# Optimization experiments

Hardware: AMD Instinct MI355X
Metric: run time of the kernel (lower is better)

## Reference

```python
import jax, jax.numpy as jnp
import numpy as np

NUM_HEADS = 16
LN_EPS = 1e-5
RMS_EPS = 1e-6


def rmsnorm(x, gamma, eps=RMS_EPS):
    xf = x.astype(jnp.float32)
    rms = jax.lax.rsqrt(jnp.mean(xf * xf, axis=-1, keepdims=True) + eps)
    return gamma * (xf * rms).astype(x.dtype)


def layernorm(x, g, b, eps=LN_EPS):
    mu = jnp.mean(x, axis=-1, keepdims=True)
    var = jnp.mean(jnp.square(x - mu), axis=-1, keepdims=True)
    return (x - mu) * jax.lax.rsqrt(var + eps) * g + b


def setup_inputs() -> dict:
    key = jax.random.key(0)
    E = 2048
    ks = jax.random.split(key, 10)
    std = 0.02
    inp = {
        "x": jax.random.normal(ks[0], (2, 2048, E), dtype=jnp.float32),
        "Wq": jax.random.normal(ks[1], (E, E), dtype=jnp.float32) * std,
        "Wk": jax.random.normal(ks[2], (E, E), dtype=jnp.float32) * std,
        "Wv": jax.random.normal(ks[3], (E, E), dtype=jnp.float32) * std,
        "Wo": jax.random.normal(ks[4], (E, E), dtype=jnp.float32) * std,
        "ln_g": jnp.ones((E,), jnp.float32),
        "ln_b": jnp.zeros((E,), jnp.float32),
        "rms_g": jnp.ones((E,), jnp.float32),
        "mlp_W0": jax.random.normal(ks[5], (E, E), dtype=jnp.float32) * std,
        "sw_W": jax.random.normal(ks[6], (E, E), dtype=jnp.float32) * std,
        "sw_V": jax.random.normal(ks[7], (E, E), dtype=jnp.float32) * std,
        "sw_beta": jnp.ones((1,), jnp.float32),
        "mlp_rms_g": jnp.ones((E,), jnp.float32),
    }
    return inp


def reference(x, Wq, Wk, Wv, Wo, ln_g, ln_b, rms_g, mlp_W0, sw_W, sw_V, sw_beta, mlp_rms_g):
    B, S, E = x.shape
    H = NUM_HEADS
    Dh = E // H
    scale = 1.0 / (Dh ** 0.5)

    # --- MultiheadAttention (faithful to original einsum/view quirks) ---
    q = x @ Wq.T                     # (B,S,E)
    k = (x @ Wk.T) * scale
    v = x @ Wv.T
    qh = q.reshape(B, S, H, Dh)
    kh = k.reshape(B, S, H, Dh)
    scores = jnp.einsum('bthd,bshd->bhts', qh, kh)        # (B,H,T,S)
    causal = jnp.tril(jnp.ones((S, S), dtype=bool))
    scores = jnp.where(causal, scores, -jnp.inf)
    attn = jax.nn.softmax(scores, axis=-1)
    # NOTE: v is split (B,S,Dh,H) -- head/head_dim axes swapped vs q/k, as in the torch code
    vh = v.reshape(B, S, Dh, H)
    ctx = jnp.einsum('bsdh,bhts->bthd', vh, attn)          # == torch 'kjlm,kmij->kiml'
    ctx = ctx.reshape(B, S, E)                              # flatten heads-major
    ctx = layernorm(ctx, ln_g, ln_b)
    attn_out = ctx @ Wo.T

    x = x + attn_out
    x = rmsnorm(x, rms_g)

    # --- MLP: Linear -> SwiGLU -> RMSNorm, residual ---
    h = x @ mlp_W0.T
    w = h @ sw_W.T
    swish = w * jax.nn.sigmoid(sw_beta * w)
    g = swish * (h @ sw_V.T)
    mlp_out = rmsnorm(g, mlp_rms_g)
    return x + mlp_out
```

## Files before the change

kernel.cpp:

```cpp
#include <hip/hip_runtime.h>


#define B_    2
#define S_    2048
#define E_    2048
#define H_    16
#define DH    128
#define MROWS 4096
#define NEGF  (-3.0e38f)

typedef unsigned short ushort_t;
typedef unsigned int   uint_t;
typedef ushort_t us8   __attribute__((ext_vector_type(8)));
typedef ushort_t us4   __attribute__((ext_vector_type(4)));
typedef __bf16   bf16x8 __attribute__((ext_vector_type(8)));
typedef float    f32x4 __attribute__((ext_vector_type(4)));

__device__ __forceinline__ float b2f(ushort_t u) {
    uint_t x = ((uint_t)u) << 16;
    union { uint_t u; float f; } c; c.u = x; return c.f;
}
__device__ __forceinline__ ushort_t f2b(float f) {
    union { float f; uint_t u; } c; c.f = f;
    uint_t x = c.u;
    uint_t r = (x + 0x7fffu + ((x >> 16) & 1u)) >> 16;
    return (ushort_t)r;
}
__device__ __forceinline__ float fexp2(float x) {
    return __builtin_amdgcn_exp2f(x);
}

__device__ __forceinline__ void gld16(const ushort_t* g, ushort_t* l) {
    __builtin_amdgcn_global_load_lds(
        (const __attribute__((address_space(1))) void*)g,
        (__attribute__((address_space(3))) void*)l,
        16, 0, 0);
}

__global__ void probe_dtype(const ushort_t* w, int* flag) {
    __shared__ int cnt;
    if (threadIdx.x == 0) cnt = 0;
    __syncthreads();
    int c = 0;
    for (int i = threadIdx.x; i < 4096; i += 256) {
        uint_t e = (w[i] >> 7) & 0xFFu;
        if (e >= 0x84u) c++;
    }
    atomicAdd(&cnt, c);
    __syncthreads();
    if (threadIdx.x == 0) *flag = (cnt >= 8) ? 1 : 0;
}

__global__ void convert_k(const void* src, ushort_t* dst, long n, const int* flag) {
    int f = *flag;
    long i0 = (long)blockIdx.x * blockDim.x + threadIdx.x;
    long stride = (long)gridDim.x * blockDim.x;
    long n4 = n >> 2;
    if (f) {
        const f32x4* s = (const f32x4*)src;
        for (long i = i0; i < n4; i += stride) {
            f32x4 v = s[i];
            us4 o = { f2b(v[0]), f2b(v[1]), f2b(v[2]), f2b(v[3]) };
            *(us4*)(dst + i * 4) = o;
        }
        for (long i = n4 * 4 + i0; i < n; i += stride)
            dst[i] = f2b(((const float*)src)[i]);
    } else {
        const us4* s = (const us4*)src;
        for (long i = i0; i < n4; i += stride)
            *(us4*)(dst + i * 4) = s[i];
        for (long i = n4 * 4 + i0; i < n; i += stride)
            dst[i] = ((const ushort_t*)src)[i];
    }
}

__global__ void fill_diag(float* out, long n, float val) {
    long i = (long)blockIdx.x * 256 + threadIdx.x;
    if (i < n) out[i] = val;
}

__global__ __launch_bounds__(256) void gemm_bt(
    const ushort_t* __restrict__ A, const ushort_t* __restrict__ W,
    ushort_t* out, const ushort_t* resid, const ushort_t* beta,
    void* outv, const int* flagp, float scale, int mode)
{
    const int K = E_, N = E_;
    __shared__ alignas(16) ushort_t Asf[128 * 32];
    __shared__ alignas(16) ushort_t Bsf[128 * 32];

    const int tid  = threadIdx.x;
    const int wave = tid >> 6;
    const int lane = tid & 63;
    const int wm   = (wave >> 1) * 64;
    const int wn   = (wave & 1) * 64;
    const int lrow = lane & 15;
    const int quad = lane >> 4;
    const int m0   = blockIdx.y * 128;
    const int n0   = blockIdx.x * 128;

    const float betav = (beta != nullptr) ? b2f(beta[0]) : 0.0f;
    const int   of32  = (flagp != nullptr) ? *flagp : 0;

    f32x4 acc[4][4];
#pragma unroll
    for (int i = 0; i < 4; i++)
#pragma unroll
        for (int j = 0; j < 4; j++) acc[i][j] = f32x4{0.f, 0.f, 0.f, 0.f};

    const int ch   = wave * 2;
    const int crow = lane >> 2;
    const int ccol = (lane & 3) * 8;
    const ushort_t* Ag0 = A + (long)(m0 + ch * 16 + crow) * K + ccol;
    const ushort_t* Wg0 = W + (long)(n0 + ch * 16 + crow) * K + ccol;
    ushort_t* Al0 = &Asf[ch * 16 * 32];
    ushort_t* Bl0 = &Bsf[ch * 16 * 32];

    for (int kk = 0; kk < K; kk += 32) {
        gld16(Ag0 + kk,          Al0);
        gld16(Ag0 + 16 * K + kk, Al0 + 512);
        gld16(Wg0 + kk,          Bl0);
        gld16(Wg0 + 16 * K + kk, Bl0 + 512);
        __syncthreads();

        bf16x8 af[4], bfr[4];
#pragma unroll
        for (int i = 0; i < 4; i++)
            af[i]  = __builtin_bit_cast(bf16x8, *(const us8*)&Asf[(wm + i*16 + lrow) * 32 + quad * 8]);
#pragma unroll
        for (int j = 0; j < 4; j++)
            bfr[j] = __builtin_bit_cast(bf16x8, *(const us8*)&Bsf[(wn + j*16 + lrow) * 32 + quad * 8]);
#pragma unroll
        for (int i = 0; i < 4; i++)
#pragma unroll
            for (int j = 0; j < 4; j++)
                acc[i][j] = __builtin_amdgcn_mfma_f32_16x16x32_bf16(af[i], bfr[j], acc[i][j], 0, 0, 0);
        __syncthreads();
    }

#pragma unroll
    for (int i = 0; i < 4; i++)
#pragma unroll
        for (int j = 0; j < 4; j++)
#pragma unroll
            for (int r = 0; r < 4; r++) {
                int m = m0 + wm + i*16 + quad*4 + r;
                int n = n0 + wn + j*16 + lrow;
                float v = acc[i][j][r] * scale;
                long idx;
                if (mode == 1) {
                    int h = n >> 7, d = n & 127;
                    idx = ((long)h * S_ + m) * DH + d;
                } else if (mode == 2) {
                    int d = n >> 4, h = n & 15;
                    idx = ((long)h * DH + d) * S_ + m;
                } else {
                    idx = (long)m * N + n;
                    if (mode == 3) {
                        v += b2f(resid[idx]);
                    } else if (mode == 4) {
                        float wv  = b2f(resid[idx]);
                        float sig = 1.0f / (1.0f + expf(-betav * wv));
                        v = wv * sig * v;
                        if (of32) { ((float*)outv)[idx] = v; continue; }
                    }
                }
                out[idx] = f2b(v);
            }
}

__global__ __launch_bounds__(256) void gemm_qkv(
    const ushort_t* __restrict__ X,
    const ushort_t* __restrict__ Wq, const ushort_t* __restrict__ Wk,
    const ushort_t* __restrict__ Wv,
    ushort_t* qo, ushort_t* ko, ushort_t* vo, float kscale)
{
    const int K = E_;
    __shared__ alignas(16) ushort_t Asf[128 * 32];
    __shared__ alignas(16) ushort_t Bsf[128 * 32];

    const int tid  = threadIdx.x;
    const int wave = tid >> 6;
    const int lane = tid & 63;
    const int wm   = (wave >> 1) * 64;
    const int wn   = (wave & 1) * 64;
    const int lrow = lane & 15;
    const int quad = lane >> 4;
    const int sel  = blockIdx.x >> 4;
    const int n0   = (blockIdx.x & 15) * 128;
    const int m0   = blockIdx.y * 128;
    const long zoff = (long)blockIdx.z * ((long)S_ * E_);

    const ushort_t* A = X + zoff;
    const ushort_t* W = (sel == 0) ? Wq : (sel == 1) ? Wk : Wv;
    const float scale = (sel == 1) ? kscale : 1.0f;
    ushort_t* out = ((sel == 0) ? qo : (sel == 1) ? ko : vo) + zoff;

    f32x4 acc[4][4];
#pragma unroll
    for (int i = 0; i < 4; i++)
#pragma unroll
        for (int j = 0; j < 4; j++) acc[i][j] = f32x4{0.f, 0.f, 0.f, 0.f};

    const int ch   = wave * 2;
    const int crow = lane >> 2;
    const int ccol = (lane & 3) * 8;
    const ushort_t* Ag0 = A + (long)(m0 + ch * 16 + crow) * K + ccol;
    const ushort_t* Wg0 = W + (long)(n0 + ch * 16 + crow) * K + ccol;
    ushort_t* Al0 = &Asf[ch * 16 * 32];
    ushort_t* Bl0 = &Bsf[ch * 16 * 32];

    for (int kk = 0; kk < K; kk += 32) {
        gld16(Ag0 + kk,          Al0);
        gld16(Ag0 + 16 * K + kk, Al0 + 512);
        gld16(Wg0 + kk,          Bl0);
        gld16(Wg0 + 16 * K + kk, Bl0 + 512);
        __syncthreads();

        bf16x8 af[4], bfr[4];
#pragma unroll
        for (int i = 0; i < 4; i++)
            af[i]  = __builtin_bit_cast(bf16x8, *(const us8*)&Asf[(wm + i*16 + lrow) * 32 + quad * 8]);
#pragma unroll
        for (int j = 0; j < 4; j++)
            bfr[j] = __builtin_bit_cast(bf16x8, *(const us8*)&Bsf[(wn + j*16 + lrow) * 32 + quad * 8]);
#pragma unroll
        for (int i = 0; i < 4; i++)
#pragma unroll
            for (int j = 0; j < 4; j++)
                acc[i][j] = __builtin_amdgcn_mfma_f32_16x16x32_bf16(af[i], bfr[j], acc[i][j], 0, 0, 0);
        __syncthreads();
    }

#pragma unroll
    for (int i = 0; i < 4; i++)
#pragma unroll
        for (int j = 0; j < 4; j++)
#pragma unroll
            for (int r = 0; r < 4; r++) {
                int m = m0 + wm + i*16 + quad*4 + r;
                int n = n0 + wn + j*16 + lrow;
                float v = acc[i][j][r] * scale;
                long idx;
                if (sel <= 1) {
                    int h = n >> 7, d = n & 127;
                    idx = ((long)h * S_ + m) * DH + d;
                } else {
                    int d = n >> 4, h = n & 15;
                    idx = ((long)h * DH + d) * S_ + m;
                }
                out[idx] = f2b(v);
            }
}

__global__ __launch_bounds__(256) void flash_attn(
    const ushort_t* __restrict__ qp, const ushort_t* __restrict__ kp,
    const ushort_t* __restrict__ vt, ushort_t* ctx)
{
    __shared__ alignas(16) ushort_t Kt[64][144];
    __shared__ alignas(16) ushort_t Vt[128][72];
    __shared__ alignas(16) ushort_t Pb[4][16][72];

    const long zq = (long)blockIdx.z * ((long)S_ * E_);
    qp  += zq; kp += zq; vt += zq; ctx += zq;

    const int tid  = threadIdx.x;
    const int wave = tid >> 6;
    const int lane = tid & 63;
    const int lrow = lane & 15;
    const int quad = lane >> 4;
    const int h    = blockIdx.y;

    const long qbase = (long)h * S_ * DH;
    const long vbase = (long)h * DH * S_;

    int kr[4], kc[4], vr[4], vc[4];
#pragma unroll
    for (int it = 0; it < 4; it++) {
        int L = tid + it * 256;
        kr[it] = L >> 4; kc[it] = (L & 15) * 8;
        vr[it] = L >> 3; vc[it] = (L & 7) * 8;
    }

#pragma unroll 1
    for (int half = 0; half < 2; half++) {
        const int qt = (half == 0) ? (int)blockIdx.x : (31 - (int)blockIdx.x);
        const int tw = qt * 64 + wave * 16;

        bf16x8 qf[4];
        {
            const ushort_t* qrow = qp + qbase + (long)(tw + lrow) * DH + quad * 8;
#pragma unroll
            for (int ks = 0; ks < 4; ks++)
                qf[ks] = __builtin_bit_cast(bf16x8, *(const us8*)(qrow + ks * 32));
        }

        float m_i[4], l_i[4];
#pragma unroll
        for (int r = 0; r < 4; r++) { m_i[r] = NEGF; l_i[r] = 0.0f; }
        f32x4 o[8];
#pragma unroll
        for (int i = 0; i < 8; i++) o[i] = f32x4{0.f, 0.f, 0.f, 0.f};

        us8 kreg[4], vreg[4];
#pragma unroll
        for (int it = 0; it < 4; it++)
            kreg[it] = *(const us8*)(kp + qbase + (long)kr[it] * DH + kc[it]);
#pragma unroll
        for (int it = 0; it < 4; it++)
            vreg[it] = *(const us8*)(vt + vbase + (long)vr[it] * S_ + vc[it]);

        for (int st = 0; st <= qt; st++) {
            const int sb = st * 64;

#pragma unroll
            for (int it = 0; it < 4; it++) *(us8*)&Kt[kr[it]][kc[it]] = kreg[it];
#pragma unroll
            for (int it = 0; it < 4; it++) *(us8*)&Vt[vr[it]][vc[it]] = vreg[it];
            __syncthreads();

            if (st < qt) {
                const int sb2 = sb + 64;
#pragma unroll
                for (int it = 0; it < 4; it++)
                    kreg[it] = *(const us8*)(kp + qbase + (long)(sb2 + kr[it]) * DH + kc[it]);
#pragma unroll
                for (int it = 0; it < 4; it++)
                    vreg[it] = *(const us8*)(vt + vbase + (long)vr[it] * S_ + sb2 + vc[it]);
            }

            f32x4 sacc[4];
#pragma unroll
            for (int nt = 0; nt < 4; nt++) {
                sacc[nt] = f32x4{0.f, 0.f, 0.f, 0.f};
#pragma unroll
                for (int ks = 0; ks < 4; ks++) {
                    bf16x8 kf = __builtin_bit_cast(bf16x8, *(const us8*)&Kt[nt*16 + lrow][ks*32 + quad*8]);
                    sacc[nt] = __builtin_amdgcn_mfma_f32_16x16x32_bf16(qf[ks], kf, sacc[nt], 0, 0, 0);
                }
            }

            const bool diag = (st == qt);
            float alpha[4];
#pragma unroll
            for (int r = 0; r < 4; r++) {
                const int trow = tw + quad * 4 + r;
                float pv[4];
#pragma unroll
                for (int nt = 0; nt < 4; nt++) {
                    float sv = sacc[nt][r];
                    if (diag && (sb + nt*16 + lrow > trow)) sv = NEGF;
                    pv[nt] = sv;
                }
                float mx = fmaxf(fmaxf(pv[0], pv[1]), fmaxf(pv[2], pv[3]));
                mx = fmaxf(mx, __shfl_xor(mx, 1));
                mx = fmaxf(mx, __shfl_xor(mx, 2));
                mx = fmaxf(mx, __shfl_xor(mx, 4));
                mx = fmaxf(mx, __shfl_xor(mx, 8));
                float mn = fmaxf(m_i[r], mx);
                float al = fexp2(m_i[r] - mn);
                float s  = 0.0f;
#pragma unroll
                for (int nt = 0; nt < 4; nt++) {
                    float p = fexp2(pv[nt] - mn);
                    s += p;
                    Pb[wave][quad*4 + r][nt*16 + lrow] = f2b(p);
                }
                s += __shfl_xor(s, 1);
                s += __shfl_xor(s, 2);
                s += __shfl_xor(s, 4);
                s += __shfl_xor(s, 8);
                l_i[r]  = l_i[r] * al + s;
                m_i[r]  = mn;
                alpha[r] = al;
            }
#pragma unroll
            for (int nt = 0; nt < 8; nt++)
#pragma unroll
                for (int r = 0; r < 4; r++) o[nt][r] *= alpha[r];

            bf16x8 pf[2];
#pragma unroll
            for (int ks = 0; ks < 2; ks++)
                pf[ks] = __builtin_bit_cast(bf16x8, *(const us8*)&Pb[wave][lrow][ks*32 + quad*8]);
#pragma unroll
            for (int nt = 0; nt < 8; nt++)
#pragma unroll
                for (int ks = 0; ks < 2; ks++) {
                    bf16x8 vf = __builtin_bit_cast(bf16x8, *(const us8*)&Vt[nt*16 + lrow][ks*32 + quad*8]);
                    o[nt] = __builtin_amdgcn_mfma_f32_16x16x32_bf16(pf[ks], vf, o[nt], 0, 0, 0);
                }
            __syncthreads();
        }

        float li4[4];
#pragma unroll
        for (int r = 0; r < 4; r++) li4[r] = 1.0f / l_i[r];
#pragma unroll
        for (int nt = 0; nt < 8; nt++)
#pragma unroll
            for (int r = 0; r < 4; r++) {
                int t = tw + quad*4 + r;
                int d = nt*16 + lrow;
                ctx[(long)t * E_ + h * DH + d] = f2b(o[nt][r] * li4[r]);
            }
    }
}

__global__ __launch_bounds__(256) void ln_rows(
    const ushort_t* x, const ushort_t* __restrict__ g,
    const ushort_t* __restrict__ bta, ushort_t* out)
{
    __shared__ float red[16];
    const int row = blockIdx.x;
    const ushort_t* xr = x + (long)row * E_;
    float vals[8], s = 0.f, ss = 0.f;
#pragma unroll
    for (int i = 0; i < 8; i++) {
        float v = b2f(xr[threadIdx.x + i * 256]);
        vals[i] = v; s += v; ss += v * v;
    }
    for (int off = 1; off < 64; off <<= 1) { s += __shfl_xor(s, off); ss += __shfl_xor(ss, off); }
    int wave = threadIdx.x >> 6, lane = threadIdx.x & 63;
    if (lane == 0) { red[wave] = s; red[8 + wave] = ss; }
    __syncthreads();
    if (threadIdx.x == 0) {
        red[4]  = red[0] + red[1] + red[2] + red[3];
        red[12] = red[8] + red[9] + red[10] + red[11];
    }
    __syncthreads();
    float mu  = red[4] / E_;
    float var = red[12] / E_ - mu * mu;
    float rs  = rsqrtf(var + 1e-5f);
#pragma unroll
    for (int i = 0; i < 8; i++) {
        int c = threadIdx.x + i * 256;
        float v = (vals[i] - mu) * rs * b2f(g[c]) + b2f(bta[c]);
        out[(long)row * E_ + c] = f2b(v);
    }
}

__global__ __launch_bounds__(256) void rms_rows(
    const ushort_t* x, const ushort_t* __restrict__ g, ushort_t* out)
{
    __shared__ float red[8];
    const int row = blockIdx.x;
    const ushort_t* xr = x + (long)row * E_;
    float vals[8], ss = 0.f;
#pragma unroll
    for (int i = 0; i < 8; i++) {
        float v = b2f(xr[threadIdx.x + i * 256]);
        vals[i] = v; ss += v * v;
    }
    for (int off = 1; off < 64; off <<= 1) ss += __shfl_xor(ss, off);
    int wave = threadIdx.x >> 6, lane = threadIdx.x & 63;
    if (lane == 0) red[wave] = ss;
    __syncthreads();
    if (threadIdx.x == 0) red[4] = red[0] + red[1] + red[2] + red[3];
    __syncthreads();
    float rms = rsqrtf(red[4] / E_ + 1e-6f);
#pragma unroll
    for (int i = 0; i < 8; i++) {
        int c = threadIdx.x + i * 256;
        float v = b2f(f2b(vals[i] * rms)) * b2f(g[c]);
        out[(long)row * E_ + c] = f2b(v);
    }
}

__global__ __launch_bounds__(256) void rms_final(
    const void* x, const ushort_t* __restrict__ g,
    const ushort_t* resid, void* outv, const int* flagp)
{
    __shared__ float red[8];
    const int row = blockIdx.x;
    const int of32 = *flagp;
    float vals[8], ss = 0.f;
#pragma unroll
    for (int i = 0; i < 8; i++) {
        int c = threadIdx.x + i * 256;
        float v = of32 ? ((const float*)x)[(long)row * E_ + c]
                       : b2f(((const ushort_t*)x)[(long)row * E_ + c]);
        vals[i] = v; ss += v * v;
    }
    for (int off = 1; off < 64; off <<= 1) ss += __shfl_xor(ss, off);
    int wave = threadIdx.x >> 6, lane = threadIdx.x & 63;
    if (lane == 0) red[wave] = ss;
    __syncthreads();
    if (threadIdx.x == 0) red[4] = red[0] + red[1] + red[2] + red[3];
    __syncthreads();
    float rms = rsqrtf(red[4] / E_ + 1e-6f);
#pragma unroll
    for (int i = 0; i < 8; i++) {
        int c = threadIdx.x + i * 256;
        long idx = (long)row * E_ + c;
        if (of32) {
            float v = vals[i] * rms * b2f(g[c]) + b2f(resid[idx]);
            ((float*)outv)[idx] = v;
        } else {
            float v = b2f(f2b(vals[i] * rms)) * b2f(g[c]) + b2f(resid[idx]);
            ((ushort_t*)outv)[idx] = f2b(v);
        }
    }
}

extern "C" void kernel_launch(void* const* d_in, const int* in_sizes, int n_in,
                              void* d_out, int out_size, void* d_ws, size_t ws_size,
                              hipStream_t stream)
{
    const size_t NB  = (size_t)MROWS * E_;
    const size_t WSZ = (size_t)E_ * E_;
    const size_t QSZ = (size_t)S_ * E_;
    const float kscale = 0.08838834764831845f * 1.4426950408889634f;

    const size_t stage_elems = NB + 7 * WSZ + 6 * 4096;
    const size_t need_def    = (stage_elems + 2 * NB) * 2;
    const size_t need_direct = 2 * NB * 2;

    dim3 gFull(E_ / 128, MROWS / 128);

    if (ws_size >= need_def) {
        ushort_t* st = (ushort_t*)d_ws;
        ushort_t* c_x   = st;
        ushort_t* c_Wq  = c_x  + NB;
        ushort_t* c_Wk  = c_Wq + WSZ;
        ushort_t* c_Wv  = c_Wk + WSZ;
        ushort_t* c_Wo  = c_Wv + WSZ;
        ushort_t* c_W0  = c_Wo + WSZ;
        ushort_t* c_sW  = c_W0 + WSZ;
        ushort_t* c_sV  = c_sW + WSZ;
        ushort_t* c_lng = c_sV + WSZ;
        ushort_t* c_lnb = c_lng + 4096;
        ushort_t* c_rg  = c_lnb + 4096;
        ushort_t* c_mg  = c_rg  + 4096;
        ushort_t* c_sb  = c_mg  + 4096;
        int*      flag  = (int*)(c_sb + 4096);
        ushort_t* w0    = st + stage_elems;
        ushort_t* w1    = w0 + NB;
        ushort_t* ob    = (ushort_t*)d_out;
        ushort_t* ob2   = ob + NB;

        probe_dtype<<<1, 256, 0, stream>>>((const ushort_t*)d_in[1], flag);
        convert_k<<<1024, 256, 0, stream>>>(d_in[0],  c_x,  (long)NB,  flag);
        convert_k<<<1024, 256, 0, stream>>>(d_in[1],  c_Wq, (long)WSZ, flag);
        convert_k<<<1024, 256, 0, stream>>>(d_in[2],  c_Wk, (long)WSZ, flag);
        convert_k<<<1024, 256, 0, stream>>>(d_in[3],  c_Wv, (long)WSZ, flag);
        convert_k<<<1024, 256, 0, stream>>>(d_in[4],  c_Wo, (long)WSZ, flag);
        convert_k<<<1024, 256, 0, stream>>>(d_in[8],  c_W0, (long)WSZ, flag);
        convert_k<<<1024, 256, 0, stream>>>(d_in[9],  c_sW, (long)WSZ, flag);
        convert_k<<<1024, 256, 0, stream>>>(d_in[10], c_sV, (long)WSZ, flag);
        convert_k<<<8,    256, 0, stream>>>(d_in[5],  c_lng, E_, flag);
        convert_k<<<8,    256, 0, stream>>>(d_in[6],  c_lnb, E_, flag);
        convert_k<<<8,    256, 0, stream>>>(d_in[7],  c_rg,  E_, flag);
        convert_k<<<8,    256, 0, stream>>>(d_in[12], c_mg,  E_, flag);
        convert_k<<<1,    64,  0, stream>>>(d_in[11], c_sb,  1,  flag);

        gemm_qkv<<<dim3(48, 16, 2), 256, 0, stream>>>(c_x, c_Wq, c_Wk, c_Wv,
                                                      w0, ob, w1, kscale);
        flash_attn<<<dim3(16, H_, 2), 256, 0, stream>>>(w0, ob, w1, ob2);

        ln_rows<<<MROWS, 256, 0, stream>>>(ob2, c_lng, c_lnb, ob2);
        gemm_bt<<<gFull, 256, 0, stream>>>(ob2, c_Wo, w1, c_x, nullptr, nullptr, nullptr, 1.0f, 3);
        rms_rows<<<MROWS, 256, 0, stream>>>(w1, c_rg, w1);
        gemm_bt<<<gFull, 256, 0, stream>>>(w1, c_W0, w0, nullptr, nullptr, nullptr, nullptr, 1.0f, 0);
        gemm_bt<<<gFull, 256, 0, stream>>>(w0, c_sW, c_x, nullptr, nullptr, nullptr, nullptr, 1.0f, 0);
        gemm_bt<<<gFull, 256, 0, stream>>>(w0, c_sV, (ushort_t*)d_out, c_x, c_sb, d_out, flag, 1.0f, 4);
        rms_final<<<MROWS, 256, 0, stream>>>(d_out, c_mg, w1, d_out, flag);
    } else if (ws_size >= need_direct) {
        ushort_t* w0 = (ushort_t*)d_ws;
        ushort_t* w1 = w0 + NB;
        ushort_t* ob = (ushort_t*)d_out;
        int* flag = (int*)((char*)d_ws + 2 * NB * 2);
        hipMemsetAsync(flag, 0, sizeof(int), stream);
        const ushort_t* x   = (const ushort_t*)d_in[0];
        const ushort_t* Wq  = (const ushort_t*)d_in[1];
        const ushort_t* Wk  = (const ushort_t*)d_in[2];
        const ushort_t* Wv  = (const ushort_t*)d_in[3];
        const ushort_t* Wo  = (const ushort_t*)d_in[4];
        const ushort_t* lng = (const ushort_t*)d_in[5];
        const ushort_t* lnb = (const ushort_t*)d_in[6];
        const ushort_t* rg  = (const ushort_t*)d_in[7];
        const ushort_t* W0  = (const ushort_t*)d_in[8];
        const ushort_t* sW  = (const ushort_t*)d_in[9];
        const ushort_t* sV  = (const ushort_t*)d_in[10];
        const ushort_t* sb  = (const ushort_t*)d_in[11];
        const ushort_t* mg  = (const ushort_t*)d_in[12];
        for (int b = 0; b < B_; b++) {
            const ushort_t* xb = x + (size_t)b * QSZ;
            gemm_qkv<<<dim3(48, 16, 1), 256, 0, stream>>>(xb, Wq, Wk, Wv,
                                                          w0, w0 + QSZ, w1, kscale);
            flash_attn<<<dim3(16, H_, 1), 256, 0, stream>>>(w0, w0 + QSZ, w1, ob + (size_t)b * QSZ);
        }
        ln_rows<<<MROWS, 256, 0, stream>>>(ob, lng, lnb, ob);
        gemm_bt<<<gFull, 256, 0, stream>>>(ob, Wo, w0, x, nullptr, nullptr, nullptr, 1.0f, 3);
        rms_rows<<<MROWS, 256, 0, stream>>>(w0, rg, w0);
        gemm_bt<<<gFull, 256, 0, stream>>>(w0, W0, w1, nullptr, nullptr, nullptr, nullptr, 1.0f, 0);
        gemm_bt<<<gFull, 256, 0, stream>>>(w1, sW, ob, nullptr, nullptr, nullptr, nullptr, 1.0f, 0);
        gemm_bt<<<gFull, 256, 0, stream>>>(w1, sV, ob, ob, sb, d_out, flag, 1.0f, 4);
        rms_final<<<MROWS, 256, 0, stream>>>(ob, mg, w0, d_out, flag);
    } else {
        fill_diag<<<((long)NB + 255) / 256, 256, 0, stream>>>((float*)d_out, (long)NB,
                                                              1000.0f + ws_size * 1e-6f);
    }
}
```

Before: 704.4 us.

## Triple-buffer GEMM K-loop with async prefetch, merge SwiGLU GEMMs and conversions

Replaces the single-buffered GEMM main loop with a shared core that keeps three LDS stages and issues global-to-LDS loads two steps ahead, using vmcnt waits and one barrier per step. The goal is to hide load latency behind MFMA work. The two SwiGLU GEMMs now run as one launch with a z selector, and the swish gating moves into a fused epilogue in the final RMSNorm kernel. The many per-tensor conversion launches collapse into two kernels. Tripling LDS may lower occupancy, and the extra sW GEMM output now goes through memory before the fused RMSNorm.

```diff
diff --git a/kernel.cpp b/kernel.cpp
--- a/kernel.cpp
+++ b/kernel.cpp
@@ -51,32 +51,139 @@
     if (threadIdx.x == 0) *flag = (cnt >= 8) ? 1 : 0;
 }
 
+__global__ void convert_all(
+    const void* sx, const void* s1, const void* s2, const void* s3,
+    const void* s4, const void* s5, const void* s6, const void* s7,
+    ushort_t* dst, const int* flagp)
+{
+    const long NBL  = (long)MROWS * E_;
+    const long WSZL = (long)E_ * E_;
+    const int f = *flagp;
+    long i0 = (long)blockIdx.x * blockDim.x + threadIdx.x;
+    long stride = (long)gridDim.x * blockDim.x;
+    const long n4 = (NBL + 7 * WSZL) >> 2;
+    for (long i = i0; i < n4; i += stride) {
+        long e = i << 2;
+        const void* s; long off;
+        if (e < NBL) { s = sx; off = e; }
+        else {
+            long r = e - NBL;
+            int j = (int)(r >> 22);
+            off = r & 0x3FFFFFL;
+            s = (j == 0) ? s1 : (j == 1) ? s2 : (j == 2) ? s3 : (j == 3) ? s4
+              : (j == 4) ? s5 : (j == 5) ? s6 : s7;
+        }
+        if (f) {
+            f32x4 v = *(const f32x4*)((const float*)s + off);
+            us4 o = { f2b(v[0]), f2b(v[1]), f2b(v[2]), f2b(v[3]) };
+            *(us4*)(dst + e) = o;
+        } else {
+            *(us4*)(dst + e) = *(const us4*)((const ushort_t*)s + off);
+        }
+    }
+}
+
+__global__ void convert_vecs(
+    const void* s0, const void* s1, const void* s2, const void* s3,
+    const void* s4, ushort_t* dstbase, const int* flagp)
+{
+    const int b = blockIdx.x;
+    const void* s = (b == 0) ? s0 : (b == 1) ? s1 : (b == 2) ? s2
+                  : (b == 3) ? s3 : s4;
+    ushort_t* d = dstbase + (long)b * 4096;
+    const int n = (b == 4) ? 1 : E_;
+    const int f = *flagp;
+    for (int i = threadIdx.x; i < n; i += 256)
+        d[i] = f ? f2b(((const float*)s)[i]) : ((const ushort_t*)s)[i];
+}
+
 __global__ void convert_k(const void* src, ushort_t* dst, long n, const int* flag) {
     int f = *flag;
     long i0 = (long)blockIdx.x * blockDim.x + threadIdx.x;
     long stride = (long)gridDim.x * blockDim.x;
-    long n4 = n >> 2;
     if (f) {
-        const f32x4* s = (const f32x4*)src;
-        for (long i = i0; i < n4; i += stride) {
-            f32x4 v = s[i];
-            us4 o = { f2b(v[0]), f2b(v[1]), f2b(v[2]), f2b(v[3]) };
-            *(us4*)(dst + i * 4) = o;
-        }
-        for (long i = n4 * 4 + i0; i < n; i += stride)
-            dst[i] = f2b(((const float*)src)[i]);
+        const float* s = (const float*)src;
+        for (long i = i0; i < n; i += stride) dst[i] = f2b(s[i]);
     } else {
-        const us4* s = (const us4*)src;
-        for (long i = i0; i < n4; i += stride)
-            *(us4*)(dst + i * 4) = s[i];
-        for (long i = n4 * 4 + i0; i < n; i += stride)
-            dst[i] = ((const ushort_t*)src)[i];
+        const ushort_t* s = (const ushort_t*)src;
+        for (long i = i0; i < n; i += stride) dst[i] = s[i];
     }
 }
 
 __global__ void fill_diag(float* out, long n, float val) {
     long i = (long)blockIdx.x * 256 + threadIdx.x;
     if (i < n) out[i] = val;
+}
+
+#define GEMM_LDS __shared__ ushort_t Ls[3][2][4096]
+
+__device__ __forceinline__ void gemm_core(
+    const ushort_t* __restrict__ A, const ushort_t* __restrict__ W,
+    int m0, int n0, int K, ushort_t (*Ls)[2][4096], f32x4 acc[4][4])
+{
+    const int tid  = threadIdx.x;
+    const int wave = tid >> 6;
+    const int lane = tid & 63;
+    const int lrow = lane & 15;
+    const int quad = lane >> 4;
+    const int wm   = (wave >> 1) * 64;
+    const int wn   = (wave & 1) * 64;
+
+#pragma unroll
+    for (int i = 0; i < 4; i++)
+#pragma unroll
+        for (int j = 0; j < 4; j++) acc[i][j] = f32x4{0.f, 0.f, 0.f, 0.f};
+
+    const int srow = wave * 16 + (lane >> 2);
+    const int scol = (lane & 3) * 8;
+    const ushort_t* Ag = A + (long)(m0 + srow) * K + scol;
+    const ushort_t* Wg = W + (long)(n0 + srow) * K + scol;
+    const int ldsb = wave * 16 * 32;
+
+    const int nk = K >> 5;
+#pragma unroll
+    for (int p = 0; p < 2; p++) {
+        const int kk = p * 32;
+        gld16(Ag + kk,               &Ls[p][0][ldsb]);
+        gld16(Ag + (long)64*K + kk,  &Ls[p][0][ldsb + 2048]);
+        gld16(Wg + kk,               &Ls[p][1][ldsb]);
+        gld16(Wg + (long)64*K + kk,  &Ls[p][1][ldsb + 2048]);
+    }
+    __builtin_amdgcn_sched_barrier(0);
+
+    int cur = 0, nxt = 2;
+    for (int t = 0; t < nk; t++) {
+        asm volatile("s_waitcnt vmcnt(4)" ::: "memory");
+        __builtin_amdgcn_s_barrier();
+        __builtin_amdgcn_sched_barrier(0);
+
+        const ushort_t* As = &Ls[cur][0][0];
+        const ushort_t* Bs = &Ls[cur][1][0];
+        bf16x8 af[4], bfr[4];
+#pragma unroll
+        for (int i = 0; i < 4; i++)
+            af[i]  = __builtin_bit_cast(bf16x8, *(const us8*)&As[(wm + i*16 + lrow) * 32 + quad * 8]);
+#pragma unroll
+        for (int j = 0; j < 4; j++)
+            bfr[j] = __builtin_bit_cast(bf16x8, *(const us8*)&Bs[(wn + j*16 + lrow) * 32 + quad * 8]);
+#pragma unroll
+        for (int i = 0; i < 4; i++)
+#pragma unroll
+            for (int j = 0; j < 4; j++)
+                acc[i][j] = __builtin_amdgcn_mfma_f32_16x16x32_bf16(af[i], bfr[j], acc[i][j], 0, 0, 0);
+
+        {
+            int tt = t + 2; if (tt > nk - 1) tt = nk - 1;
+            const int kk = tt * 32;
+            gld16(Ag + kk,              &Ls[nxt][0][ldsb]);
+            gld16(Ag + (long)64*K + kk, &Ls[nxt][0][ldsb + 2048]);
+            gld16(Wg + kk,              &Ls[nxt][1][ldsb]);
+            gld16(Wg + (long)64*K + kk, &Ls[nxt][1][ldsb + 2048]);
+        }
+        __builtin_amdgcn_sched_barrier(0);
+        cur = (cur == 2) ? 0 : cur + 1;
+        nxt = (nxt == 2) ? 0 : nxt + 1;
+    }
 }
 
 __global__ __launch_bounds__(256) void gemm_bt(
@@ -85,16 +192,14 @@
     void* outv, const int* flagp, float scale, int mode)
 {
     const int K = E_, N = E_;
-    __shared__ alignas(16) ushort_t Asf[128 * 32];
-    __shared__ alignas(16) ushort_t Bsf[128 * 32];
-
+    GEMM_LDS;
     const int tid  = threadIdx.x;
     const int wave = tid >> 6;
     const int lane = tid & 63;
+    const int lrow = lane & 15;
+    const int quad = lane >> 4;
     const int wm   = (wave >> 1) * 64;
     const int wn   = (wave & 1) * 64;
-    const int lrow = lane & 15;
-    const int quad = lane >> 4;
     const int m0   = blockIdx.y * 128;
     const int n0   = blockIdx.x * 128;
 
@@ -102,40 +207,7 @@
     const int   of32  = (flagp != nullptr) ? *flagp : 0;
 
     f32x4 acc[4][4];
-#pragma unroll
-    for (int i = 0; i < 4; i++)
-#pragma unroll
-        for (int j = 0; j < 4; j++) acc[i][j] = f32x4{0.f, 0.f, 0.f, 0.f};
-
-    const int ch   = wave * 2;
-    const int crow = lane >> 2;
-    const int ccol = (lane & 3) * 8;
-    const ushort_t* Ag0 = A + (long)(m0 + ch * 16 + crow) * K + ccol;
-    const ushort_t* Wg0 = W + (long)(n0 + ch * 16 + crow) * K + ccol;
-    ushort_t* Al0 = &Asf[ch * 16 * 32];
-    ushort_t* Bl0 = &Bsf[ch * 16 * 32];
-
-    for (int kk = 0; kk < K; kk += 32) {
-        gld16(Ag0 + kk,          Al0);
-        gld16(Ag0 + 16 * K + kk, Al0 + 512);
-        gld16(Wg0 + kk,          Bl0);
-        gld16(Wg0 + 16 * K + kk, Bl0 + 512);
-        __syncthreads();
-
-        bf16x8 af[4], bfr[4];
-#pragma unroll
-        for (int i = 0; i < 4; i++)
-            af[i]  = __builtin_bit_cast(bf16x8, *(const us8*)&Asf[(wm + i*16 + lrow) * 32 + quad * 8]);
-#pragma unroll
-        for (int j = 0; j < 4; j++)
-            bfr[j] = __builtin_bit_cast(bf16x8, *(const us8*)&Bsf[(wn + j*16 + lrow) * 32 + quad * 8]);
-#pragma unroll
-        for (int i = 0; i < 4; i++)
-#pragma unroll
-            for (int j = 0; j < 4; j++)
-                acc[i][j] = __builtin_amdgcn_mfma_f32_16x16x32_bf16(af[i], bfr[j], acc[i][j], 0, 0, 0);
-        __syncthreads();
-    }
+    gemm_core(A, W, m0, n0, K, Ls, acc);
 
 #pragma unroll
     for (int i = 0; i < 4; i++)
@@ -175,16 +247,14 @@
     ushort_t* qo, ushort_t* ko, ushort_t* vo, float kscale)
 {
     const int K = E_;
-    __shared__ alignas(16) ushort_t Asf[128 * 32];
-    __shared__ alignas(16) ushort_t Bsf[128 * 32];
-
+    GEMM_LDS;
     const int tid  = threadIdx.x;
     const int wave = tid >> 6;
     const int lane = tid & 63;
+    const int lrow = lane & 15;
+    const int quad = lane >> 4;
     const int wm   = (wave >> 1) * 64;
     const int wn   = (wave & 1) * 64;
-    const int lrow = lane & 15;
-    const int quad = lane >> 4;
     const int sel  = blockIdx.x >> 4;
     const int n0   = (blockIdx.x & 15) * 128;
     const int m0   = blockIdx.y * 128;
@@ -196,40 +266,7 @@
     ushort_t* out = ((sel == 0) ? qo : (sel == 1) ? ko : vo) + zoff;
 
     f32x4 acc[4][4];
-#pragma unroll
-    for (int i = 0; i < 4; i++)
-#pragma unroll
-        for (int j = 0; j < 4; j++) acc[i][j] = f32x4{0.f, 0.f, 0.f, 0.f};
-
-    const int ch   = wave * 2;
-    const int crow = lane >> 2;
-    const int ccol = (lane & 3) * 8;
-    const ushort_t* Ag0 = A + (long)(m0 + ch * 16 + crow) * K + ccol;
-    const ushort_t* Wg0 = W + (long)(n0 + ch * 16 + crow) * K + ccol;
-    ushort_t* Al0 = &Asf[ch * 16 * 32];
-    ushort_t* Bl0 = &Bsf[ch * 16 * 32];
-
-    for (int kk = 0; kk < K; kk += 32) {
-        gld16(Ag0 + kk,          Al0);
-        gld16(Ag0 + 16 * K + kk, Al0 + 512);
-        gld16(Wg0 + kk,          Bl0);
-        gld16(Wg0 + 16 * K + kk, Bl0 + 512);
-        __syncthreads();
-
-        bf16x8 af[4], bfr[4];
-#pragma unroll
-        for (int i = 0; i < 4; i++)
-            af[i]  = __builtin_bit_cast(bf16x8, *(const us8*)&Asf[(wm + i*16 + lrow) * 32 + quad * 8]);
-#pragma unroll
-        for (int j = 0; j < 4; j++)
-            bfr[j] = __builtin_bit_cast(bf16x8, *(const us8*)&Bsf[(wn + j*16 + lrow) * 32 + quad * 8]);
-#pragma unroll
-        for (int i = 0; i < 4; i++)
-#pragma unroll
-            for (int j = 0; j < 4; j++)
-                acc[i][j] = __builtin_amdgcn_mfma_f32_16x16x32_bf16(af[i], bfr[j], acc[i][j], 0, 0, 0);
-        __syncthreads();
-    }
+    gemm_core(A, W, m0, n0, K, Ls, acc);
 
 #pragma unroll
     for (int i = 0; i < 4; i++)
@@ -252,6 +289,45 @@
             }
 }
 
+__global__ __launch_bounds__(256) void gemm_pair(
+    const ushort_t* __restrict__ A,
+    const ushort_t* __restrict__ Wa, const ushort_t* __restrict__ Wb,
+    ushort_t* outa, void* outb, const int* flagp)
+{
+    const int K = E_, N = E_;
+    GEMM_LDS;
+    const int tid  = threadIdx.x;
+    const int wave = tid >> 6;
+    const int lane = tid & 63;
+    const int lrow = lane & 15;
+    const int quad = lane >> 4;
+    const int wm   = (wave >> 1) * 64;
+    const int wn   = (wave & 1) * 64;
+    const int m0   = blockIdx.y * 128;
+    const int n0   = blockIdx.x * 128;
+    const int sel  = blockIdx.z;
+    const int of32 = *flagp;
+
+    const ushort_t* W = sel ? Wb : Wa;
+    f32x4 acc[4][4];
+    gemm_core(A, W, m0, n0, K, Ls, acc);
+
+#pragma unroll
+    for (int i = 0; i < 4; i++)
+#pragma unroll
+        for (int j = 0; j < 4; j++)
+#pragma unroll
+            for (int r = 0; r < 4; r++) {
+                int m = m0 + wm + i*16 + quad*4 + r;
+                int n = n0 + wn + j*16 + lrow;
+                long idx = (long)m * N + n;
+                float v = acc[i][j][r];
+                if (sel == 0)           outa[idx] = f2b(v);
+                else if (of32)          ((float*)outb)[idx] = v;
+                else                    ((ushort_t*)outb)[idx] = f2b(v);
+            }
+}
+
 __global__ __launch_bounds__(256) void flash_attn(
     const ushort_t* __restrict__ qp, const ushort_t* __restrict__ kp,
     const ushort_t* __restrict__ vt, ushort_t* ctx)
@@ -463,6 +539,47 @@
         int c = threadIdx.x + i * 256;
         float v = b2f(f2b(vals[i] * rms)) * b2f(g[c]);
         out[(long)row * E_ + c] = f2b(v);
+    }
+}
+
+__global__ __launch_bounds__(256) void rms_final_swiglu(
+    const ushort_t* __restrict__ w, const void* y,
+    const ushort_t* __restrict__ g, const ushort_t* resid,
+    const ushort_t* beta, void* outv, const int* flagp)
+{
+    __shared__ float red[8];
+    const int row = blockIdx.x;
+    const int of32 = *flagp;
+    const float betav = b2f(beta[0]);
+    float vals[8], ss = 0.f;
+#pragma unroll
+    for (int i = 0; i < 8; i++) {
+        int c = threadIdx.x + i * 256;
+        long idx = (long)row * E_ + c;
+        float wv = b2f(w[idx]);
+        float yv = of32 ? ((const float*)y)[idx] : b2f(((const ushort_t*)y)[idx]);
+        float sig = 1.0f / (1.0f + expf(-betav * wv));
+        float gv = wv * sig * yv;
+        vals[i] = gv; ss += gv * gv;
+    }
+    for (int off = 1; off < 64; off <<= 1) ss += __shfl_xor(ss, off);
+    int wave = threadIdx.x >> 6, lane = threadIdx.x & 63;
+    if (lane == 0) red[wave] = ss;
+    __syncthreads();
+    if (threadIdx.x == 0) red[4] = red[0] + red[1] + red[2] + red[3];
+    __syncthreads();
+    float rms = rsqrtf(red[4] / E_ + 1e-6f);
+#pragma unroll
+    for (int i = 0; i < 8; i++) {
+        int c = threadIdx.x + i * 256;
+        long idx = (long)row * E_ + c;
+        if (of32) {
+            float v = vals[i] * rms * b2f(g[c]) + b2f(resid[idx]);
+            ((float*)outv)[idx] = v;
+        } else {
+            float v = b2f(f2b(vals[i] * rms)) * b2f(g[c]) + b2f(resid[idx]);
+            ((ushort_t*)outv)[idx] = f2b(v);
+        }
     }
 }
 
@@ -539,19 +656,11 @@
         ushort_t* ob2   = ob + NB;
 
         probe_dtype<<<1, 256, 0, stream>>>((const ushort_t*)d_in[1], flag);
-        convert_k<<<1024, 256, 0, stream>>>(d_in[0],  c_x,  (long)NB,  flag);
-        convert_k<<<1024, 256, 0, stream>>>(d_in[1],  c_Wq, (long)WSZ, flag);
-        convert_k<<<1024, 256, 0, stream>>>(d_in[2],  c_Wk, (long)WSZ, flag);
-        convert_k<<<1024, 256, 0, stream>>>(d_in[3],  c_Wv, (long)WSZ, flag);
-        convert_k<<<1024, 256, 0, stream>>>(d_in[4],  c_Wo, (long)WSZ, flag);
-        convert_k<<<1024, 256, 0, stream>>>(d_in[8],  c_W0, (long)WSZ, flag);
-        convert_k<<<1024, 256, 0, stream>>>(d_in[9],  c_sW, (long)WSZ, flag);
-        convert_k<<<1024, 256, 0, stream>>>(d_in[10], c_sV, (long)WSZ, flag);
-        convert_k<<<8,    256, 0, stream>>>(d_in[5],  c_lng, E_, flag);
-        convert_k<<<8,    256, 0, stream>>>(d_in[6],  c_lnb, E_, flag);
-        convert_k<<<8,    256, 0, stream>>>(d_in[7],  c_rg,  E_, flag);
-        convert_k<<<8,    256, 0, stream>>>(d_in[12], c_mg,  E_, flag);
-        convert_k<<<1,    64,  0, stream>>>(d_in[11], c_sb,  1,  flag);
+        convert_all<<<2048, 256, 0, stream>>>(d_in[0], d_in[1], d_in[2], d_in[3],
+                                              d_in[4], d_in[8], d_in[9], d_in[10],
+                                              st, flag);
+        convert_vecs<<<5, 256, 0, stream>>>(d_in[5], d_in[6], d_in[7], d_in[12],
+                                            d_in[11], c_lng, flag);
 
         gemm_qkv<<<dim3(48, 16, 2), 256, 0, stream>>>(c_x, c_Wq, c_Wk, c_Wv,
                                                       w0, ob, w1, kscale);
@@ -561,9 +670,8 @@
         gemm_bt<<<gFull, 256, 0, stream>>>(ob2, c_Wo, w1, c_x, nullptr, nullptr, nullptr, 1.0f, 3);
         rms_rows<<<MROWS, 256, 0, stream>>>(w1, c_rg, w1);
         gemm_bt<<<gFull, 256, 0, stream>>>(w1, c_W0, w0, nullptr, nullptr, nullptr, nullptr, 1.0f, 0);
-        gemm_bt<<<gFull, 256, 0, stream>>>(w0, c_sW, c_x, nullptr, nullptr, nullptr, nullptr, 1.0f, 0);
-        gemm_bt<<<gFull, 256, 0, stream>>>(w0, c_sV, (ushort_t*)d_out, c_x, c_sb, d_out, flag, 1.0f, 4);
-        rms_final<<<MROWS, 256, 0, stream>>>(d_out, c_mg, w1, d_out, flag);
+        gemm_pair<<<dim3(16, 32, 2), 256, 0, stream>>>(w0, c_sW, c_sV, c_x, d_out, flag);
+        rms_final_swiglu<<<MROWS, 256, 0, stream>>>(c_x, d_out, c_mg, w1, c_sb, d_out, flag);
     } else if (ws_size >= need_direct) {
         ushort_t* w0 = (ushort_t*)d_ws;
         ushort_t* w1 = w0 + NB;
```

Result: faster. 658.2 us (-6.6%).
